# Kernel optimization log

Hardware: AMD Instinct MI355X
Metric: run time of the kernel (lower is better)

## Reference

```python
import jax, jax.numpy as jnp
import numpy as np

B, H, L, D = 4, 16, 2048, 128


def setup_inputs() -> dict:
    key = jax.random.key(0)
    kx, kw1, kb1, kw2, kb2 = jax.random.split(key, 5)
    s = 1.0 / np.sqrt(D)
    return {
        "x": jax.random.normal(kx, (B, H, L, D), dtype=jnp.float32),
        "W1": jax.random.uniform(kw1, (D, D), jnp.float32, -s, s),
        "b1": jax.random.uniform(kb1, (D,), jnp.float32, -s, s),
        "W2": jax.random.uniform(kw2, (D, D), jnp.float32, -s, s),
        "b2": jax.random.uniform(kb2, (D,), jnp.float32, -s, s),
    }


def reference(x, W1, b1, W2, b2):
    # proj_1/proj_2: Linear(dim, dim) on the last axis (torch stores W as [out,in])
    q = jnp.einsum('bhld,ed->bhle', x, W1) + b1  # [B,H,L,D]
    k = jnp.einsum('bhld,ed->bhle', x, W2) + b2  # [B,H,L,D]
    # exact-erf GELU on raw QK^T scores, then softmax over j
    adj = jax.nn.gelu(jnp.einsum('bhid,bhjd->bhij', q, k), approximate=False)
    adj = jax.nn.softmax(adj, axis=-1)  # [B,H,L,L]
    # dropout is identity in eval mode
    out = jnp.einsum('bhij,bhjd->bhid', adj, x)  # [B,H,L,D]
    return out.transpose(0, 2, 1, 3).reshape(B, L, H * D)
```

## Files before the change

kernel.cpp:

```cpp
#include <hip/hip_runtime.h>
#include <hip/hip_bf16.h>

#define B_ 4
#define H_ 16
#define L_ 2048
#define D_ 128
#define BH_ 64

typedef __attribute__((ext_vector_type(8))) _Float16 f16x8;
typedef __attribute__((ext_vector_type(4))) float f32x4;
typedef __attribute__((ext_vector_type(16))) float f32x16;
typedef __attribute__((ext_vector_type(2))) unsigned u32x2;

#define L2E 1.44269504088896f

__device__ __forceinline__ float gelu_m(float v, float negm) {
  float x  = __builtin_fabsf(v) * 0.70710678118f;
  float s  = __builtin_fmaf(x,
               __builtin_fmaf(x,
                 __builtin_fmaf(x,
                   __builtin_fmaf(x, 0.078108f, 0.000972f),
                 0.230389f),
               0.278393f),
             1.0f);
  float s2 = s * s;
  float s4 = s2 * s2;
  float erfa = 1.0f - __builtin_amdgcn_rcpf(s4);
  float erfv = copysignf(erfa, v);
  float hv   = 0.72134752f * v;
  return __builtin_fmaf(hv, erfv, hv + negm);
}

__device__ __forceinline__ void gl2lds16(const void* g, void* l) {
  __builtin_amdgcn_global_load_lds(
      (const __attribute__((address_space(1))) void*)g,
      (__attribute__((address_space(3))) void*)l, 16, 0, 0);
}

__device__ __forceinline__ unsigned pkrtz(float a, float b) {
  auto t = __builtin_amdgcn_cvt_pkrtz(a, b);
  return __builtin_bit_cast(unsigned, t);
}

__global__ __launch_bounds__(256) void wcvt_kernel(
    const float* __restrict__ W1, const float* __restrict__ W2,
    _Float16* __restrict__ Wh1, _Float16* __restrict__ Wh2)
{
  int i = blockIdx.x * 256 + threadIdx.x;
  Wh1[i] = (_Float16)W1[i];
  Wh2[i] = (_Float16)W2[i];
}

__global__ __launch_bounds__(256) void proj_tr_kernel(
    const float* __restrict__ x,
    const _Float16* __restrict__ Wh1, const float* __restrict__ b1,
    const _Float16* __restrict__ Wh2, const float* __restrict__ b2,
    _Float16* __restrict__ Qb, _Float16* __restrict__ Kb,
    _Float16* __restrict__ VT)
{
  const int tid  = threadIdx.x;
  const int wave = tid >> 6;
  const int lane = tid & 63;
  const int lhi  = lane >> 4;
  const int llo  = lane & 15;
  const int r0   = blockIdx.x * 64;
  const int wr0  = r0 + wave * 16;

  f16x8 a[4];
#pragma unroll
  for (int ks = 0; ks < 4; ++ks) {
    const float* p = x + (size_t)(wr0 + llo) * D_ + lhi * 8 + ks * 32;
    f16x8 t;
#pragma unroll
    for (int e = 0; e < 8; ++e) t[e] = (_Float16)p[e];
    a[ks] = t;
  }

  f32x4 accq[8], acck[8];
#pragma unroll
  for (int n = 0; n < 8; ++n) {
    accq[n] = (f32x4){0.f, 0.f, 0.f, 0.f};
    acck[n] = (f32x4){0.f, 0.f, 0.f, 0.f};
  }

#pragma unroll
  for (int n = 0; n < 8; ++n) {
    const int e = n * 16 + llo;
#pragma unroll
    for (int ks = 0; ks < 4; ++ks) {
      f16x8 w1f = *(const f16x8*)(Wh1 + (size_t)e * D_ + lhi * 8 + ks * 32);
      f16x8 w2f = *(const f16x8*)(Wh2 + (size_t)e * D_ + lhi * 8 + ks * 32);
      accq[n] = __builtin_amdgcn_mfma_f32_16x16x32_f16(a[ks], w1f, accq[n], 0, 0, 0);
      acck[n] = __builtin_amdgcn_mfma_f32_16x16x32_f16(a[ks], w2f, acck[n], 0, 0, 0);
    }
  }

#pragma unroll
  for (int n = 0; n < 8; ++n) {
    const int e = n * 16 + llo;
    const float bias1 = b1[e];
    const float bias2 = b2[e];
#pragma unroll
    for (int r = 0; r < 4; ++r) {
      const size_t row = (size_t)wr0 + lhi * 4 + r;
      Qb[row * D_ + e] = (_Float16)(accq[n][r] + bias1);
      Kb[row * D_ + e] = (_Float16)(acck[n][r] + bias2);
    }
  }

  const int bh = r0 / L_;
  const int l0 = r0 % L_;
  const int d  = tid & 127;
  const int rh = tid >> 7;
  _Float16* dst = VT + (size_t)bh * D_ * L_ + (size_t)d * L_ + l0 + rh * 32;
#pragma unroll
  for (int j = 0; j < 4; ++j) {
    f16x8 t;
#pragma unroll
    for (int e = 0; e < 8; ++e)
      t[e] = (_Float16)x[(size_t)(r0 + rh * 32 + j * 8 + e) * D_ + d];
    *(f16x8*)(dst + j * 8) = t;
  }
}

__global__ __launch_bounds__(512) void attn_kernel(
    const _Float16* __restrict__ Qb, const _Float16* __restrict__ Kb,
    const _Float16* __restrict__ VT, float* __restrict__ out)
{
  __shared__ _Float16 Ks[2][64 * 128];
  __shared__ _Float16 Vs[2][128 * 128];

  const int tid  = threadIdx.x;
  const int wave = tid >> 6;
  const int lane = tid & 63;
  const int l5   = lane & 31;
  const int hi   = lane >> 5;

  const int bid = blockIdx.x;
  const int blk = (bid & 7) * 64 + (bid >> 3);
  const int bh  = blk >> 3;
  const int q0  = (blk & 7) * 256;
  const int b   = bh >> 4;
  const int h   = bh & 15;
  const int wq0 = q0 + wave * 32;

  const char* KheadB = (const char*)(Kb + (size_t)bh * L_ * D_);
  const char* VheadB = (const char*)(VT + (size_t)bh * D_ * L_);

  int kdst[2], ksrc[2];
#pragma unroll
  for (int c = 0; c < 2; ++c) {
    const int wc = wave * 2 + c;
    kdst[c] = wc * 1024;
    const int l  = wc * 4 + (lane >> 4);
    const int c0 = (lane & 15) * 8;
    ksrc[c] = l * 256 + 2 * (c0 ^ ((l & 15) << 3));
  }
  int vdst[4], vsrc[4];
#pragma unroll
  for (int c = 0; c < 4; ++c) {
    vdst[c] = c * 8192 + wave * 1024;
    const int d  = c * 32 + wave * 4 + (lane >> 4);
    const int c0 = (lane & 15) * 8;
    vsrc[c] = d * 4096 + 2 * (c0 ^ ((d & 15) << 3));
  }
  const int swz4 = (l5 & 15) << 3;

  f16x8 qf[8];
#pragma unroll
  for (int s = 0; s < 8; ++s)
    qf[s] = *(const f16x8*)(Qb + ((size_t)bh * L_ + wq0 + l5) * D_ + s * 16 + hi * 8);

  f32x16 accO[4];
#pragma unroll
  for (int n = 0; n < 4; ++n)
#pragma unroll
    for (int r = 0; r < 16; ++r) accO[n][r] = 0.f;
  float negm = 64.f;
  float l = 0.f;

#pragma unroll
  for (int c = 0; c < 2; ++c)
    gl2lds16(KheadB + ksrc[c], (char*)&Ks[0][0] + kdst[c]);
#pragma unroll
  for (int c = 0; c < 4; ++c)
    gl2lds16(VheadB + vsrc[c], (char*)&Vs[0][0] + vdst[c]);
  __syncthreads();

  for (int t = 0; t < L_ / 64; ++t) {
    const int kcur = t & 1;
    const int vcur = (t >> 1) & 1;
    if (t + 1 < L_ / 64) {
      const char* kt_ = KheadB + (size_t)(t + 1) * 64 * 256;
#pragma unroll
      for (int c = 0; c < 2; ++c)
        gl2lds16(kt_ + ksrc[c], (char*)&Ks[kcur ^ 1][0] + kdst[c]);
    }
    if ((t & 1) == 0 && (t >> 1) + 1 < L_ / 128) {
      const char* vt_ = VheadB + (size_t)((t >> 1) + 1) * 256;
#pragma unroll
      for (int c = 0; c < 4; ++c)
        gl2lds16(vt_ + vsrc[c], (char*)&Vs[vcur ^ 1][0] + vdst[c]);
    }
    const _Float16* Kcur = &Ks[kcur][0];
    const _Float16* Vcur = &Vs[vcur][0];
    const int vt0 = (t & 1) * 64;

    f32x16 sA, sB;
#pragma unroll
    for (int r = 0; r < 16; ++r) { sA[r] = 0.f; sB[r] = 0.f; }
    __builtin_amdgcn_s_setprio(1);
#pragma unroll
    for (int s = 0; s < 8; ++s) {
      f16x8 kfa = *(const f16x8*)(Kcur + l5 * 128 +
                                  ((s * 16 + hi * 8) ^ swz4));
      sA = __builtin_amdgcn_mfma_f32_32x32x16_f16(kfa, qf[s], sA, 0, 0, 0);
      f16x8 kfb = *(const f16x8*)(Kcur + (32 + l5) * 128 +
                                  ((s * 16 + hi * 8) ^ swz4));
      sB = __builtin_amdgcn_mfma_f32_32x32x16_f16(kfb, qf[s], sB, 0, 0, 0);
    }
    __builtin_amdgcn_s_setprio(0);

    auto softmax_pv = [&](const f32x16& sT, int vkbase) {
      float gm[16];
#pragma unroll
      for (int r = 0; r < 16; ++r) gm[r] = gelu_m(sT[r], negm);

      float tm = fmaxf(fmaxf(gm[0], gm[1]), gm[2]);
      tm = fmaxf(fmaxf(tm, gm[3]),  gm[4]);
      tm = fmaxf(fmaxf(tm, gm[5]),  gm[6]);
      tm = fmaxf(fmaxf(tm, gm[7]),  gm[8]);
      tm = fmaxf(fmaxf(tm, gm[9]),  gm[10]);
      tm = fmaxf(fmaxf(tm, gm[11]), gm[12]);
      tm = fmaxf(fmaxf(tm, gm[13]), gm[14]);
      tm = fmaxf(tm, gm[15]);
      tm = fmaxf(tm, __shfl_xor(tm, 32));

      float p[16];
      float ts;
      if (__all(tm <= 11.5415603f)) {
#pragma unroll
        for (int r = 0; r < 16; ++r) p[r] = __builtin_amdgcn_exp2f(gm[r]);
        float a0 = p[0]+p[1],   a1 = p[2]+p[3],   a2 = p[4]+p[5],   a3 = p[6]+p[7];
        float a4 = p[8]+p[9],   a5 = p[10]+p[11], a6 = p[12]+p[13], a7 = p[14]+p[15];
        ts = ((a0+a1)+(a2+a3)) + ((a4+a5)+(a6+a7));
        ts += __shfl_xor(ts, 32);
        l += ts;
      } else {
        float dm = fmaxf(tm, 0.f);
        negm -= dm;
        float sc = __builtin_amdgcn_exp2f(-dm);
#pragma unroll
        for (int r = 0; r < 16; ++r) p[r] = __builtin_amdgcn_exp2f(gm[r] - dm);
        float a0 = p[0]+p[1],   a1 = p[2]+p[3],   a2 = p[4]+p[5],   a3 = p[6]+p[7];
        float a4 = p[8]+p[9],   a5 = p[10]+p[11], a6 = p[12]+p[13], a7 = p[14]+p[15];
        ts = ((a0+a1)+(a2+a3)) + ((a4+a5)+(a6+a7));
        ts += __shfl_xor(ts, 32);
        l = __builtin_fmaf(l, sc, ts);
        float scr[16];
#pragma unroll
        for (int r = 0; r < 16; ++r)
          scr[r] = __shfl(sc, (r & 3) + 8 * (r >> 2) + 4 * hi);
#pragma unroll
        for (int n = 0; n < 4; ++n)
#pragma unroll
          for (int r = 0; r < 16; ++r) accO[n][r] *= scr[r];
      }

      unsigned pk01 = pkrtz(p[0], p[1]),   pk23 = pkrtz(p[2], p[3]);
      unsigned pk45 = pkrtz(p[4], p[5]),   pk67 = pkrtz(p[6], p[7]);
      unsigned pk89 = pkrtz(p[8], p[9]),   pkAB = pkrtz(p[10], p[11]);
      unsigned pkCD = pkrtz(p[12], p[13]), pkEF = pkrtz(p[14], p[15]);
      u32x2 r0 = __builtin_amdgcn_permlane32_swap(pk01, pk45, false, false);
      u32x2 r1 = __builtin_amdgcn_permlane32_swap(pk23, pk67, false, false);
      u32x2 r2 = __builtin_amdgcn_permlane32_swap(pk89, pkCD, false, false);
      u32x2 r3 = __builtin_amdgcn_permlane32_swap(pkAB, pkEF, false, false);
      union { unsigned u[4]; f16x8 v; } A0c, A1c;
      A0c.u[0] = r0[0]; A0c.u[1] = r1[0]; A0c.u[2] = r0[1]; A0c.u[3] = r1[1];
      A1c.u[0] = r2[0]; A1c.u[1] = r3[0]; A1c.u[2] = r2[1]; A1c.u[3] = r3[1];

      __builtin_amdgcn_s_setprio(1);
#pragma unroll
      for (int n = 0; n < 4; ++n) {
        f16x8 vf0 = *(const f16x8*)(Vcur + (n * 32 + l5) * 128 +
                                    ((vkbase + hi * 8) ^ swz4));
        accO[n] = __builtin_amdgcn_mfma_f32_32x32x16_f16(A0c.v, vf0, accO[n], 0, 0, 0);
        f16x8 vf1 = *(const f16x8*)(Vcur + (n * 32 + l5) * 128 +
                                    ((vkbase + 16 + hi * 8) ^ swz4));
        accO[n] = __builtin_amdgcn_mfma_f32_32x32x16_f16(A1c.v, vf1, accO[n], 0, 0, 0);
      }
      __builtin_amdgcn_s_setprio(0);
    };

    softmax_pv(sA, vt0);
    softmax_pv(sB, vt0 + 32);

    __syncthreads();
  }

  float linv = __builtin_amdgcn_rcpf(l);
  float lb[16];
#pragma unroll
  for (int r = 0; r < 16; ++r)
    lb[r] = __shfl(linv, (r & 3) + 8 * (r >> 2) + 4 * hi);
#pragma unroll
  for (int n = 0; n < 4; ++n)
#pragma unroll
    for (int r = 0; r < 16; ++r) {
      const int i = wq0 + (r & 3) + 8 * (r >> 2) + 4 * hi;
      out[((size_t)(b * L_ + i) * H_ + h) * D_ + n * 32 + l5] = accO[n][r] * lb[r];
    }
}

extern "C" void kernel_launch(void* const* d_in, const int* in_sizes, int n_in,
                              void* d_out, int out_size, void* d_ws, size_t ws_size,
                              hipStream_t stream) {
  const float* x  = (const float*)d_in[0];
  const float* W1 = (const float*)d_in[1];
  const float* b1 = (const float*)d_in[2];
  const float* W2 = (const float*)d_in[3];
  const float* b2 = (const float*)d_in[4];
  float* out = (float*)d_out;

  const size_t N = (size_t)BH_ * L_ * D_;
  _Float16* Qb = (_Float16*)d_ws;
  _Float16* Kb = Qb + N;
  _Float16* VT = Kb + N;

  _Float16* Wh1 = (_Float16*)d_out;
  _Float16* Wh2 = Wh1 + D_ * D_;

  wcvt_kernel<<<64, 256, 0, stream>>>(W1, W2, Wh1, Wh2);
  proj_tr_kernel<<<(BH_ * L_) / 64, 256, 0, stream>>>(x, Wh1, b1, Wh2, b2, Qb, Kb, VT);
  attn_kernel<<<BH_ * (L_ / 256), 512, 0, stream>>>(Qb, Kb, VT, out);
}
```

Before: 378.7 us.

## Software-pipeline QK^T one tile ahead of softmax and PV

Restructures the main loop so the QK^T MFMAs for the next K tile are issued before the GELU/softmax/PV work of the current tile. Score accumulators are double-buffered and the loop is unrolled by two. The aim is to overlap matrix-core work with the VALU-heavy GELU/exp phase within a wave. In exchange it holds two more f32x16 accumulators in registers, which may raise VGPR pressure or cause spills, and the buffer reuse is tied to the new barrier placement.

```diff
diff --git a/kernel.cpp b/kernel.cpp
--- a/kernel.cpp
+++ b/kernel.cpp
@@ -179,122 +179,131 @@
   float negm = 64.f;
   float l = 0.f;
 
-#pragma unroll
-  for (int c = 0; c < 2; ++c)
-    gl2lds16(KheadB + ksrc[c], (char*)&Ks[0][0] + kdst[c]);
-#pragma unroll
-  for (int c = 0; c < 4; ++c)
-    gl2lds16(VheadB + vsrc[c], (char*)&Vs[0][0] + vdst[c]);
+  auto stageK = [&](int tile) {
+    const char* kt_ = KheadB + (size_t)tile * 64 * 256;
+    char* dst = (char*)&Ks[tile & 1][0];
+#pragma unroll
+    for (int c = 0; c < 2; ++c) gl2lds16(kt_ + ksrc[c], dst + kdst[c]);
+  };
+  auto stageV = [&](int sup) {
+    const char* vt_ = VheadB + (size_t)sup * 256;
+    char* dst = (char*)&Vs[sup & 1][0];
+#pragma unroll
+    for (int c = 0; c < 4; ++c) gl2lds16(vt_ + vsrc[c], dst + vdst[c]);
+  };
+  auto qk = [&](const _Float16* Kbuf, f32x16& dA, f32x16& dB) {
+#pragma unroll
+    for (int r = 0; r < 16; ++r) { dA[r] = 0.f; dB[r] = 0.f; }
+    __builtin_amdgcn_s_setprio(1);
+#pragma unroll
+    for (int s = 0; s < 8; ++s) {
+      f16x8 kfa = *(const f16x8*)(Kbuf + l5 * 128 + ((s * 16 + hi * 8) ^ swz4));
+      dA = __builtin_amdgcn_mfma_f32_32x32x16_f16(kfa, qf[s], dA, 0, 0, 0);
+      f16x8 kfb = *(const f16x8*)(Kbuf + (32 + l5) * 128 + ((s * 16 + hi * 8) ^ swz4));
+      dB = __builtin_amdgcn_mfma_f32_32x32x16_f16(kfb, qf[s], dB, 0, 0, 0);
+    }
+    __builtin_amdgcn_s_setprio(0);
+  };
+  auto softmax_pv = [&](const f32x16& sT, const _Float16* Vcur, int vkbase) {
+    float gm[16];
+#pragma unroll
+    for (int r = 0; r < 16; ++r) gm[r] = gelu_m(sT[r], negm);
+
+    float tm = fmaxf(fmaxf(gm[0], gm[1]), gm[2]);
+    tm = fmaxf(fmaxf(tm, gm[3]),  gm[4]);
+    tm = fmaxf(fmaxf(tm, gm[5]),  gm[6]);
+    tm = fmaxf(fmaxf(tm, gm[7]),  gm[8]);
+    tm = fmaxf(fmaxf(tm, gm[9]),  gm[10]);
+    tm = fmaxf(fmaxf(tm, gm[11]), gm[12]);
+    tm = fmaxf(fmaxf(tm, gm[13]), gm[14]);
+    tm = fmaxf(tm, gm[15]);
+    tm = fmaxf(tm, __shfl_xor(tm, 32));
+
+    float p[16];
+    float ts;
+    if (__all(tm <= 11.5415603f)) {
+#pragma unroll
+      for (int r = 0; r < 16; ++r) p[r] = __builtin_amdgcn_exp2f(gm[r]);
+      float a0 = p[0]+p[1],   a1 = p[2]+p[3],   a2 = p[4]+p[5],   a3 = p[6]+p[7];
+      float a4 = p[8]+p[9],   a5 = p[10]+p[11], a6 = p[12]+p[13], a7 = p[14]+p[15];
+      ts = ((a0+a1)+(a2+a3)) + ((a4+a5)+(a6+a7));
+      ts += __shfl_xor(ts, 32);
+      l += ts;
+    } else {
+      float dm = fmaxf(tm, 0.f);
+      negm -= dm;
+      float sc = __builtin_amdgcn_exp2f(-dm);
+#pragma unroll
+      for (int r = 0; r < 16; ++r) p[r] = __builtin_amdgcn_exp2f(gm[r] - dm);
+      float a0 = p[0]+p[1],   a1 = p[2]+p[3],   a2 = p[4]+p[5],   a3 = p[6]+p[7];
+      float a4 = p[8]+p[9],   a5 = p[10]+p[11], a6 = p[12]+p[13], a7 = p[14]+p[15];
+      ts = ((a0+a1)+(a2+a3)) + ((a4+a5)+(a6+a7));
+      ts += __shfl_xor(ts, 32);
+      l = __builtin_fmaf(l, sc, ts);
+      float scr[16];
+#pragma unroll
+      for (int r = 0; r < 16; ++r)
+        scr[r] = __shfl(sc, (r & 3) + 8 * (r >> 2) + 4 * hi);
+#pragma unroll
+      for (int n = 0; n < 4; ++n)
+#pragma unroll
+        for (int r = 0; r < 16; ++r) accO[n][r] *= scr[r];
+    }
+
+    unsigned pk01 = pkrtz(p[0], p[1]),   pk23 = pkrtz(p[2], p[3]);
+    unsigned pk45 = pkrtz(p[4], p[5]),   pk67 = pkrtz(p[6], p[7]);
+    unsigned pk89 = pkrtz(p[8], p[9]),   pkAB = pkrtz(p[10], p[11]);
+    unsigned pkCD = pkrtz(p[12], p[13]), pkEF = pkrtz(p[14], p[15]);
+    u32x2 r0 = __builtin_amdgcn_permlane32_swap(pk01, pk45, false, false);
+    u32x2 r1 = __builtin_amdgcn_permlane32_swap(pk23, pk67, false, false);
+    u32x2 r2 = __builtin_amdgcn_permlane32_swap(pk89, pkCD, false, false);
+    u32x2 r3 = __builtin_amdgcn_permlane32_swap(pkAB, pkEF, false, false);
+    union { unsigned u[4]; f16x8 v; } A0c, A1c;
+    A0c.u[0] = r0[0]; A0c.u[1] = r1[0]; A0c.u[2] = r0[1]; A0c.u[3] = r1[1];
+    A1c.u[0] = r2[0]; A1c.u[1] = r3[0]; A1c.u[2] = r2[1]; A1c.u[3] = r3[1];
+
+    __builtin_amdgcn_s_setprio(1);
+#pragma unroll
+    for (int n = 0; n < 4; ++n) {
+      f16x8 vf0 = *(const f16x8*)(Vcur + (n * 32 + l5) * 128 +
+                                  ((vkbase + hi * 8) ^ swz4));
+      accO[n] = __builtin_amdgcn_mfma_f32_32x32x16_f16(A0c.v, vf0, accO[n], 0, 0, 0);
+      f16x8 vf1 = *(const f16x8*)(Vcur + (n * 32 + l5) * 128 +
+                                  ((vkbase + 16 + hi * 8) ^ swz4));
+      accO[n] = __builtin_amdgcn_mfma_f32_32x32x16_f16(A1c.v, vf1, accO[n], 0, 0, 0);
+    }
+    __builtin_amdgcn_s_setprio(0);
+  };
+
+  stageK(0);
+  stageK(1);
+  stageV(0);
   __syncthreads();
-
-  for (int t = 0; t < L_ / 64; ++t) {
-    const int kcur = t & 1;
-    const int vcur = (t >> 1) & 1;
-    if (t + 1 < L_ / 64) {
-      const char* kt_ = KheadB + (size_t)(t + 1) * 64 * 256;
-#pragma unroll
-      for (int c = 0; c < 2; ++c)
-        gl2lds16(kt_ + ksrc[c], (char*)&Ks[kcur ^ 1][0] + kdst[c]);
-    }
-    if ((t & 1) == 0 && (t >> 1) + 1 < L_ / 128) {
-      const char* vt_ = VheadB + (size_t)((t >> 1) + 1) * 256;
-#pragma unroll
-      for (int c = 0; c < 4; ++c)
-        gl2lds16(vt_ + vsrc[c], (char*)&Vs[vcur ^ 1][0] + vdst[c]);
-    }
-    const _Float16* Kcur = &Ks[kcur][0];
-    const _Float16* Vcur = &Vs[vcur][0];
-    const int vt0 = (t & 1) * 64;
-
-    f32x16 sA, sB;
-#pragma unroll
-    for (int r = 0; r < 16; ++r) { sA[r] = 0.f; sB[r] = 0.f; }
-    __builtin_amdgcn_s_setprio(1);
-#pragma unroll
-    for (int s = 0; s < 8; ++s) {
-      f16x8 kfa = *(const f16x8*)(Kcur + l5 * 128 +
-                                  ((s * 16 + hi * 8) ^ swz4));
-      sA = __builtin_amdgcn_mfma_f32_32x32x16_f16(kfa, qf[s], sA, 0, 0, 0);
-      f16x8 kfb = *(const f16x8*)(Kcur + (32 + l5) * 128 +
-                                  ((s * 16 + hi * 8) ^ swz4));
-      sB = __builtin_amdgcn_mfma_f32_32x32x16_f16(kfb, qf[s], sB, 0, 0, 0);
-    }
-    __builtin_amdgcn_s_setprio(0);
-
-    auto softmax_pv = [&](const f32x16& sT, int vkbase) {
-      float gm[16];
-#pragma unroll
-      for (int r = 0; r < 16; ++r) gm[r] = gelu_m(sT[r], negm);
-
-      float tm = fmaxf(fmaxf(gm[0], gm[1]), gm[2]);
-      tm = fmaxf(fmaxf(tm, gm[3]),  gm[4]);
-      tm = fmaxf(fmaxf(tm, gm[5]),  gm[6]);
-      tm = fmaxf(fmaxf(tm, gm[7]),  gm[8]);
-      tm = fmaxf(fmaxf(tm, gm[9]),  gm[10]);
-      tm = fmaxf(fmaxf(tm, gm[11]), gm[12]);
-      tm = fmaxf(fmaxf(tm, gm[13]), gm[14]);
-      tm = fmaxf(tm, gm[15]);
-      tm = fmaxf(tm, __shfl_xor(tm, 32));
-
-      float p[16];
-      float ts;
-      if (__all(tm <= 11.5415603f)) {
-#pragma unroll
-        for (int r = 0; r < 16; ++r) p[r] = __builtin_amdgcn_exp2f(gm[r]);
-        float a0 = p[0]+p[1],   a1 = p[2]+p[3],   a2 = p[4]+p[5],   a3 = p[6]+p[7];
-        float a4 = p[8]+p[9],   a5 = p[10]+p[11], a6 = p[12]+p[13], a7 = p[14]+p[15];
-        ts = ((a0+a1)+(a2+a3)) + ((a4+a5)+(a6+a7));
-        ts += __shfl_xor(ts, 32);
-        l += ts;
-      } else {
-        float dm = fmaxf(tm, 0.f);
-        negm -= dm;
-        float sc = __builtin_amdgcn_exp2f(-dm);
-#pragma unroll
-        for (int r = 0; r < 16; ++r) p[r] = __builtin_amdgcn_exp2f(gm[r] - dm);
-        float a0 = p[0]+p[1],   a1 = p[2]+p[3],   a2 = p[4]+p[5],   a3 = p[6]+p[7];
-        float a4 = p[8]+p[9],   a5 = p[10]+p[11], a6 = p[12]+p[13], a7 = p[14]+p[15];
-        ts = ((a0+a1)+(a2+a3)) + ((a4+a5)+(a6+a7));
-        ts += __shfl_xor(ts, 32);
-        l = __builtin_fmaf(l, sc, ts);
-        float scr[16];
-#pragma unroll
-        for (int r = 0; r < 16; ++r)
-          scr[r] = __shfl(sc, (r & 3) + 8 * (r >> 2) + 4 * hi);
-#pragma unroll
-        for (int n = 0; n < 4; ++n)
-#pragma unroll
-          for (int r = 0; r < 16; ++r) accO[n][r] *= scr[r];
-      }
-
-      unsigned pk01 = pkrtz(p[0], p[1]),   pk23 = pkrtz(p[2], p[3]);
-      unsigned pk45 = pkrtz(p[4], p[5]),   pk67 = pkrtz(p[6], p[7]);
-      unsigned pk89 = pkrtz(p[8], p[9]),   pkAB = pkrtz(p[10], p[11]);
-      unsigned pkCD = pkrtz(p[12], p[13]), pkEF = pkrtz(p[14], p[15]);
-      u32x2 r0 = __builtin_amdgcn_permlane32_swap(pk01, pk45, false, false);
-      u32x2 r1 = __builtin_amdgcn_permlane32_swap(pk23, pk67, false, false);
-      u32x2 r2 = __builtin_amdgcn_permlane32_swap(pk89, pkCD, false, false);
-      u32x2 r3 = __builtin_amdgcn_permlane32_swap(pkAB, pkEF, false, false);
-      union { unsigned u[4]; f16x8 v; } A0c, A1c;
-      A0c.u[0] = r0[0]; A0c.u[1] = r1[0]; A0c.u[2] = r0[1]; A0c.u[3] = r1[1];
-      A1c.u[0] = r2[0]; A1c.u[1] = r3[0]; A1c.u[2] = r2[1]; A1c.u[3] = r3[1];
-
-      __builtin_amdgcn_s_setprio(1);
-#pragma unroll
-      for (int n = 0; n < 4; ++n) {
-        f16x8 vf0 = *(const f16x8*)(Vcur + (n * 32 + l5) * 128 +
-                                    ((vkbase + hi * 8) ^ swz4));
-        accO[n] = __builtin_amdgcn_mfma_f32_32x32x16_f16(A0c.v, vf0, accO[n], 0, 0, 0);
-        f16x8 vf1 = *(const f16x8*)(Vcur + (n * 32 + l5) * 128 +
-                                    ((vkbase + 16 + hi * 8) ^ swz4));
-        accO[n] = __builtin_amdgcn_mfma_f32_32x32x16_f16(A1c.v, vf1, accO[n], 0, 0, 0);
-      }
-      __builtin_amdgcn_s_setprio(0);
-    };
-
-    softmax_pv(sA, vt0);
-    softmax_pv(sB, vt0 + 32);
-
+  f32x16 sA, sB, s2A, s2B;
+  qk(&Ks[0][0], sA, sB);
+  __syncthreads();
+
+  for (int t = 0; t < 32; t += 2) {
+    if (t + 2 < 32) stageK(t + 2);
+    if (((t >> 1) + 1) < 16) stageV((t >> 1) + 1);
+    if (t + 1 < 32) qk(&Ks[(t + 1) & 1][0], s2A, s2B);
+    {
+      const _Float16* Vcur = &Vs[(t >> 1) & 1][0];
+      const int vt0 = (t & 1) * 64;
+      softmax_pv(sA, Vcur, vt0);
+      softmax_pv(sB, Vcur, vt0 + 32);
+    }
+    __syncthreads();
+
+    const int u = t + 1;
+    if (u + 2 < 32) stageK(u + 2);
+    if (u + 1 < 32) qk(&Ks[(u + 1) & 1][0], sA, sB);
+    {
+      const _Float16* Vcur = &Vs[(u >> 1) & 1][0];
+      const int vt0 = (u & 1) * 64;
+      softmax_pv(s2A, Vcur, vt0);
+      softmax_pv(s2B, Vcur, vt0 + 32);
+    }
     __syncthreads();
   }
 
```

Measured after the change: 599.0 us. 1.58x slower.
